# Performance work log

Measured on AMD Instinct MI355X. Metric: run time of the kernel, lower is better.

The kernel has to match this reference:

```python
import jax, jax.numpy as jnp
import numpy as np

DIM = 1024
NUM_HEADS = 16
HEAD_DIM = DIM // NUM_HEADS
EPS = 1e-6


def _xavier(key, shape, gain=0.1):
    fan_in, fan_out = shape[1], shape[0]
    limit = gain * np.sqrt(6.0 / (fan_in + fan_out))
    return jax.random.uniform(key, shape, jnp.float32, -limit, limit)


def setup_inputs() -> dict:
    key = jax.random.key(0)
    kx, kq, kk, kv, ko = jax.random.split(key, 5)
    B, N = 4, 4096
    return {
        "x": jax.random.normal(kx, (B, N, DIM), jnp.float32),
        "Wq": _xavier(kq, (DIM, DIM)), "bq": jnp.zeros((DIM,), jnp.float32),
        "Wk": _xavier(kk, (DIM, DIM)), "bk": jnp.zeros((DIM,), jnp.float32),
        "Wv": _xavier(kv, (DIM, DIM)), "bv": jnp.zeros((DIM,), jnp.float32),
        "Wo": _xavier(ko, (DIM, DIM)), "bo": jnp.zeros((DIM,), jnp.float32),
    }


def _phi(x):
    # ELU feature map: elu(x) + 1 ensures non-negativity
    return jax.nn.elu(x) + 1.0


def reference(x, Wq, bq, Wk, bk, Wv, bv, Wo, bo):
    B, N, D = x.shape
    H, Hd = NUM_HEADS, HEAD_DIM
    # torch Linear: y = x @ W.T + b
    Q = (x @ Wq.T + bq).reshape(B, N, H, Hd).transpose(0, 2, 1, 3)
    K = (x @ Wk.T + bk).reshape(B, N, H, Hd).transpose(0, 2, 1, 3)
    V = (x @ Wv.T + bv).reshape(B, N, H, Hd).transpose(0, 2, 1, 3)
    Q = _phi(Q)
    K = _phi(K)
    KV = jnp.einsum('bhnd,bhne->bhde', K, V)          # [B,H,Hd,Hd] state
    out = jnp.einsum('bhnd,bhde->bhne', Q, KV)        # [B,H,N,Hd]
    Z = K.sum(axis=2)                                  # [B,H,Hd]
    norm = jnp.einsum('bhnd,bhd->bhn', Q, Z)[..., None] + EPS
    out = out / norm
    out = out.transpose(0, 2, 1, 3).reshape(B, N, D)
    return out @ Wo.T + bo
```

## Files before the change

### kernel.cpp

```cpp
#include <hip/hip_runtime.h>
#include <math.h>

#define DIMC 1024
#define SEQ 4096
#define BATCH 4
#define NH 16
#define HD 64
#define MTOT (BATCH * SEQ)
#define NSPLIT 8
#define PELEMS (64 * 64 * 64 + 64 * 64)
#define EPS 1e-6f
#define NKT (DIMC / 64)

typedef __bf16 bf16x8 __attribute__((ext_vector_type(8)));
typedef __bf16 bf16x4 __attribute__((ext_vector_type(4)));
typedef __bf16 bf16x2 __attribute__((ext_vector_type(2)));
typedef float  f32x4  __attribute__((ext_vector_type(4)));

#define MFMA16 __builtin_amdgcn_mfma_f32_16x16x32_bf16

__device__ __forceinline__ float phi_f(float x) {
    return x > 0.0f ? x + 1.0f : __expf(x);
}

__global__ __launch_bounds__(256) void cvt_all(
    const float* __restrict__ x,
    const float* __restrict__ Wq, const float* __restrict__ Wk,
    const float* __restrict__ Wv, const float* __restrict__ Wo,
    __bf16* __restrict__ xb,
    __bf16* __restrict__ Wqb, __bf16* __restrict__ Wkb,
    __bf16* __restrict__ Wvb, __bf16* __restrict__ Wob)
{
    const size_t big = (size_t)MTOT * DIMC;
    const size_t wsz = (size_t)DIMC * DIMC;
    size_t i = ((size_t)blockIdx.x * 256 + threadIdx.x) * 4;
    const float* src; __bf16* dst; size_t off;
    if (i < big) { src = x; dst = xb; off = i; }
    else {
        size_t j = i - big;
        int w = (int)(j >> 20);
        off = j & (wsz - 1);
        switch (w) {
            case 0: src = Wq; dst = Wqb; break;
            case 1: src = Wk; dst = Wkb; break;
            case 2: src = Wv; dst = Wvb; break;
            default: src = Wo; dst = Wob; break;
        }
    }
    float4 v = *(const float4*)(src + off);
    bf16x4 o = { (__bf16)v.x, (__bf16)v.y, (__bf16)v.z, (__bf16)v.w };
    *(bf16x4*)(dst + off) = o;
}

template<int OUT_BF16>
__device__ __forceinline__ void gemm_tile256(
    const __bf16* __restrict__ X, const __bf16* __restrict__ W,
    const float* __restrict__ bias, void* __restrict__ Yv,
    int m0, int n0, int do_phi)
{
    __shared__ __attribute__((aligned(16))) __bf16 lds[65536];
    const int tid  = threadIdx.x;
    const int wave = tid >> 6, lane = tid & 63;
    const int wm = wave >> 2, wn = wave & 3;
    const int fr = lane & 15, fkb = lane >> 4;
    const int fsw = fr & 7;
    const int srow = lane >> 3;
    const int sblk = (lane & 7) ^ srow;

    const __bf16* Asrc = X + (size_t)(m0 + wave * 8 + srow) * DIMC + sblk * 8;
    const __bf16* Bsrc = W + (size_t)(n0 + wave * 8 + srow) * DIMC + sblk * 8;
    __bf16* lw = lds + wave * 512;

    auto stage = [&](int isB, int h, int kblk, int bb) {
        const __bf16* s = (isB ? Bsrc : Asrc)
                          + (size_t)(h * 128) * DIMC + (size_t)kblk * 64;
        __bf16* d = lw + bb * 32768 + isB * 16384 + h * 8192;
        #pragma unroll
        for (int g = 0; g < 2; ++g)
            __builtin_amdgcn_global_load_lds(
                (const __attribute__((address_space(1))) void*)(s + (size_t)g * 64 * DIMC),
                (__attribute__((address_space(3))) void*)(d + g * 4096),
                16, 0, 0);
    };
    auto lda = [&](int bb, int i, int ks) -> bf16x8 {
        return *(const bf16x8*)(lds + bb * 32768 + wm * 8192
                 + (i * 16 + fr) * 64 + (((ks * 4 + fkb) ^ fsw) * 8));
    };
    auto ldb = [&](int bb, int j, int ks) -> bf16x8 {
        return *(const bf16x8*)(lds + bb * 32768 + 16384 + (wn >> 1) * 8192
                 + ((wn & 1) * 64 + j * 16 + fr) * 64 + (((ks * 4 + fkb) ^ fsw) * 8));
    };

    f32x4 acc[8][4] = {};
    bf16x8 a[4][2], b[4][2];

    stage(1, 0, 0, 0); stage(1, 1, 0, 0);
    stage(0, 0, 0, 0); stage(0, 1, 0, 0);
    stage(1, 0, 1, 1); stage(1, 1, 1, 1);
    stage(0, 0, 1, 1);
    asm volatile("s_waitcnt vmcnt(6)" ::: "memory");
    __builtin_amdgcn_s_barrier();

    #pragma unroll 2
    for (int t = 0; t < NKT; ++t) {
        const int buf = t & 1;
        #pragma unroll
        for (int i = 0; i < 4; ++i)
            #pragma unroll
            for (int ks = 0; ks < 2; ++ks) a[i][ks] = lda(buf, i, ks);
        #pragma unroll
        for (int j = 0; j < 2; ++j)
            #pragma unroll
            for (int ks = 0; ks < 2; ++ks) b[j][ks] = ldb(buf, j, ks);
        if (t + 1 < NKT) stage(0, 1, t + 1, buf ^ 1);
        __builtin_amdgcn_s_barrier();
        asm volatile("s_waitcnt lgkmcnt(0)" ::: "memory");
        __builtin_amdgcn_s_setprio(1);
        #pragma unroll
        for (int i = 0; i < 4; ++i)
            #pragma unroll
            for (int j = 0; j < 2; ++j)
                #pragma unroll
                for (int ks = 0; ks < 2; ++ks)
                    acc[i][j] = MFMA16(a[i][ks], b[j][ks], acc[i][j], 0, 0, 0);
        __builtin_amdgcn_s_setprio(0);
        __builtin_amdgcn_s_barrier();
        #pragma unroll
        for (int j = 2; j < 4; ++j)
            #pragma unroll
            for (int ks = 0; ks < 2; ++ks) b[j][ks] = ldb(buf, j, ks);
        __builtin_amdgcn_s_barrier();
        asm volatile("s_waitcnt lgkmcnt(0)" ::: "memory");
        __builtin_amdgcn_s_setprio(1);
        #pragma unroll
        for (int i = 0; i < 4; ++i)
            #pragma unroll
            for (int j = 2; j < 4; ++j)
                #pragma unroll
                for (int ks = 0; ks < 2; ++ks)
                    acc[i][j] = MFMA16(a[i][ks], b[j][ks], acc[i][j], 0, 0, 0);
        __builtin_amdgcn_s_setprio(0);
        __builtin_amdgcn_s_barrier();
        #pragma unroll
        for (int i = 0; i < 4; ++i)
            #pragma unroll
            for (int ks = 0; ks < 2; ++ks) a[i][ks] = lda(buf, i + 4, ks);
        if (t + 2 < NKT) stage(1, 0, t + 2, buf);
        __builtin_amdgcn_s_barrier();
        asm volatile("s_waitcnt lgkmcnt(0)" ::: "memory");
        __builtin_amdgcn_s_setprio(1);
        #pragma unroll
        for (int i = 0; i < 4; ++i)
            #pragma unroll
            for (int j = 2; j < 4; ++j)
                #pragma unroll
                for (int ks = 0; ks < 2; ++ks)
                    acc[i + 4][j] = MFMA16(a[i][ks], b[j][ks], acc[i + 4][j], 0, 0, 0);
        __builtin_amdgcn_s_setprio(0);
        __builtin_amdgcn_s_barrier();
        if (t + 2 < NKT) {
            stage(1, 1, t + 2, buf);
            stage(0, 0, t + 2, buf);
        }
        __builtin_amdgcn_s_setprio(1);
        #pragma unroll
        for (int i = 0; i < 4; ++i)
            #pragma unroll
            for (int j = 0; j < 2; ++j)
                #pragma unroll
                for (int ks = 0; ks < 2; ++ks)
                    acc[i + 4][j] = MFMA16(a[i][ks], b[j][ks], acc[i + 4][j], 0, 0, 0);
        __builtin_amdgcn_s_setprio(0);
        if (t < NKT - 2)       asm volatile("s_waitcnt vmcnt(6)" ::: "memory");
        else if (t == NKT - 2) asm volatile("s_waitcnt vmcnt(0)" ::: "memory");
        __builtin_amdgcn_s_barrier();
    }

    const int col_l = lane & 15, quad = lane >> 4;
    const int cbase = n0 + wn * 64 + col_l;
    float bb4[4];
    #pragma unroll
    for (int j = 0; j < 4; ++j) bb4[j] = bias[cbase + j * 16];
    #pragma unroll
    for (int i = 0; i < 8; ++i) {
        #pragma unroll
        for (int r = 0; r < 4; ++r) {
            const size_t grow = (size_t)(m0 + wm * 128 + i * 16 + quad * 4 + r) * DIMC;
            #pragma unroll
            for (int j = 0; j < 4; ++j) {
                float v = acc[i][j][r] + bb4[j];
                if (do_phi) v = phi_f(v);
                if (OUT_BF16)
                    ((__bf16*)Yv)[grow + cbase + j * 16] = (__bf16)v;
                else
                    ((float*)Yv)[grow + cbase + j * 16] = v;
            }
        }
    }
}

__global__ __launch_bounds__(512, 2) void gemm_qkv(
    const __bf16* __restrict__ X,
    const __bf16* __restrict__ Wq, const __bf16* __restrict__ Wk,
    const __bf16* __restrict__ Wv,
    const float* __restrict__ bq, const float* __restrict__ bk,
    const float* __restrict__ bv,
    __bf16* __restrict__ Q, __bf16* __restrict__ K, __bf16* __restrict__ V)
{
    const int l = blockIdx.x;
    const int xcd = l & 7, s = l >> 3;
    const int mat = s >> 5;
    const int t = s & 31;
    const int nb = t & 3;
    const int m_idx = xcd * 8 + (t >> 2);
    const __bf16* W = (mat == 0) ? Wq : (mat == 1) ? Wk : Wv;
    const float* bias = (mat == 0) ? bq : (mat == 1) ? bk : bv;
    __bf16* Y = (mat == 0) ? Q : (mat == 1) ? K : V;
    gemm_tile256<1>(X, W, bias, (void*)Y, m_idx * 256, nb * 256, mat != 2);
}

__global__ __launch_bounds__(512, 2) void gemm_out(
    const __bf16* __restrict__ A, const __bf16* __restrict__ Wo,
    const float* __restrict__ bo, float* __restrict__ out)
{
    const int l = blockIdx.x;
    const int xcd = l & 7, s = l >> 3;
    const int m_idx = xcd * 8 + (s >> 2);
    const int nb = s & 3;
    gemm_tile256<0>(A, Wo, bo, (void*)out, m_idx * 256, nb * 256, 0);
}

__global__ __launch_bounds__(256) void kv_z_kernel(
    const __bf16* __restrict__ Kb, const __bf16* __restrict__ Vb,
    float* __restrict__ P)
{
    __shared__ __attribute__((aligned(16))) __bf16 Kt[2][64 * 36];
    __shared__ __attribute__((aligned(16))) __bf16 Vt[2][64 * 36];
    __shared__ float zs[64];
    const int tid = threadIdx.x, wave = tid >> 6, lane = tid & 63;
    const int bh = blockIdx.x, b = bh >> 4, h = bh & 15;
    const int split = blockIdx.y;
    const int n0 = split * (SEQ / NSPLIT);
    const int dg = (tid & 15) * 4;
    const int u2 = (tid >> 4) * 2;
    const int fr = lane & 15, fk = (lane >> 4) * 8;
    const __bf16* Kp = Kb + ((size_t)b * SEQ + n0) * DIMC + h * HD;
    const __bf16* Vp = Vb + ((size_t)b * SEQ + n0) * DIMC + h * HD;
    constexpr int CH = (SEQ / NSPLIT) / 32;

    if (tid < 64) zs[tid] = 0.0f;
    f32x4 acc[4] = {};
    float zp[4] = {};

    auto ldc = [&](int c, bf16x4& ka, bf16x4& kb, bf16x4& va, bf16x4& vb) {
        ka = *(const bf16x4*)(Kp + (size_t)(c * 32 + u2) * DIMC + dg);
        kb = *(const bf16x4*)(Kp + (size_t)(c * 32 + u2 + 1) * DIMC + dg);
        va = *(const bf16x4*)(Vp + (size_t)(c * 32 + u2) * DIMC + dg);
        vb = *(const bf16x4*)(Vp + (size_t)(c * 32 + u2 + 1) * DIMC + dg);
    };

    bf16x4 ka, kb, va, vb;
    ldc(0, ka, kb, va, vb);

    for (int c = 0; c < CH; ++c) {
        const int p = c & 1;
        #pragma unroll
        for (int q = 0; q < 4; ++q) {
            zp[q] += (float)ka[q] + (float)kb[q];
            *(bf16x2*)(Kt[p] + (dg + q) * 36 + u2) = bf16x2{ka[q], kb[q]};
            *(bf16x2*)(Vt[p] + (dg + q) * 36 + u2) = bf16x2{va[q], vb[q]};
        }
        bf16x4 nka, nkb, nva, nvb;
        if (c + 1 < CH) ldc(c + 1, nka, nkb, nva, nvb);
        __syncthreads();

        const __bf16* ar = Kt[p] + (wave * 16 + fr) * 36 + fk;
        bf16x4 alo = *(const bf16x4*)ar, ahi = *(const bf16x4*)(ar + 4);
        bf16x8 af = {alo[0],alo[1],alo[2],alo[3],ahi[0],ahi[1],ahi[2],ahi[3]};
        #pragma unroll
        for (int j = 0; j < 4; ++j) {
            const __bf16* br = Vt[p] + (j * 16 + fr) * 36 + fk;
            bf16x4 blo = *(const bf16x4*)br, bhi = *(const bf16x4*)(br + 4);
            bf16x8 bf = {blo[0],blo[1],blo[2],blo[3],bhi[0],bhi[1],bhi[2],bhi[3]};
            acc[j] = __builtin_amdgcn_mfma_f32_16x16x32_bf16(af, bf, acc[j], 0, 0, 0);
        }
        ka = nka; kb = nkb; va = nva; vb = nvb;
    }

    #pragma unroll
    for (int q = 0; q < 4; ++q) atomicAdd(&zs[dg + q], zp[q]);
    __syncthreads();

    float* KVp = P + (size_t)split * PELEMS + bh * 4096;
    const int col_l = lane & 15, quad = lane >> 4;
    #pragma unroll
    for (int j = 0; j < 4; ++j)
        #pragma unroll
        for (int r = 0; r < 4; ++r)
            KVp[(wave * 16 + quad * 4 + r) * 64 + j * 16 + col_l] = acc[j][r];
    if (tid < 64)
        P[(size_t)split * PELEMS + 64 * 64 * 64 + bh * 64 + tid] = zs[tid];
}

__global__ __launch_bounds__(256) void reduce_partials(
    const float* __restrict__ P, float* __restrict__ F)
{
    const int i = blockIdx.x * 256 + threadIdx.x;
    if (i < PELEMS) {
        float s = 0.0f;
        #pragma unroll
        for (int sp = 0; sp < NSPLIT; ++sp) s += P[(size_t)sp * PELEMS + i];
        F[i] = s;
    }
}

__global__ __launch_bounds__(256) void attn_apply(
    const __bf16* __restrict__ Qb, const float* __restrict__ KV,
    const float* __restrict__ Z, __bf16* __restrict__ Ab)
{
    __shared__ __align__(16) float KVs[64][64];
    __shared__ __align__(16) float Qs[32][64];
    __shared__ float Zs[64];
    __shared__ float rnorm[32];
    const int tid = threadIdx.x;
    const int bh = blockIdx.y;
    const int b = bh >> 4, h = bh & 15;
    const int n0 = blockIdx.x * 32;

    const float* KVp = KV + (size_t)bh * HD * HD;
    #pragma unroll
    for (int r = 0; r < 4; ++r) {
        const int idx = (r * 256 + tid) * 4;
        *(float4*)&((float*)KVs)[idx] = *(const float4*)(KVp + idx);
    }
    const __bf16* Qp = Qb + ((size_t)(b * SEQ + n0)) * DIMC + h * HD;
    {
        const int tok = tid >> 3, col = (tid & 7) * 8;
        bf16x8 q8 = *(const bf16x8*)(Qp + (size_t)tok * DIMC + col);
        #pragma unroll
        for (int q = 0; q < 8; ++q) Qs[tok][col + q] = (float)q8[q];
    }
    if (tid < 64) Zs[tid] = Z[bh * HD + tid];
    __syncthreads();

    if (tid < 32) {
        float s = 0.0f;
        #pragma unroll
        for (int d = 0; d < 64; ++d) s += Qs[tid][d] * Zs[d];
        rnorm[tid] = 1.0f / (s + EPS);
    }
    __syncthreads();

    const int trow = tid >> 3;
    const int e0 = (tid & 7) * 8;
    float out[8] = {};
    #pragma unroll
    for (int d = 0; d < 64; ++d) {
        const float q = Qs[trow][d];
        #pragma unroll
        for (int j = 0; j < 8; ++j) out[j] = fmaf(q, KVs[d][e0 + j], out[j]);
    }
    const float rn = rnorm[trow];
    __bf16* Op = Ab + ((size_t)(b * SEQ + n0 + trow)) * DIMC + h * HD + e0;
    bf16x8 o;
    #pragma unroll
    for (int j = 0; j < 8; ++j) o[j] = (__bf16)(out[j] * rn);
    *(bf16x8*)Op = o;
}

extern "C" void kernel_launch(void* const* d_in, const int* in_sizes, int n_in,
                              void* d_out, int out_size, void* d_ws, size_t ws_size,
                              hipStream_t stream) {
    const float* x  = (const float*)d_in[0];
    const float* Wq = (const float*)d_in[1];
    const float* bq = (const float*)d_in[2];
    const float* Wk = (const float*)d_in[3];
    const float* bk = (const float*)d_in[4];
    const float* Wv = (const float*)d_in[5];
    const float* bv = (const float*)d_in[6];
    const float* Wo = (const float*)d_in[7];
    const float* bo = (const float*)d_in[8];
    float* out = (float*)d_out;

    const size_t big = (size_t)MTOT * DIMC;
    const size_t wsz = (size_t)DIMC * DIMC;
    __bf16* wsp = (__bf16*)d_ws;
    __bf16* xb  = wsp;
    __bf16* Wqb = xb + big;
    __bf16* Wkb = Wqb + wsz;
    __bf16* Wvb = Wkb + wsz;
    __bf16* Wob = Wvb + wsz;
    __bf16* Qb  = Wob + wsz;
    __bf16* Kb  = Qb + big;
    __bf16* Vb  = Kb + big;
    __bf16* Ab  = xb;
    float*  P   = (float*)(Vb + big);
    float*  F   = P + (size_t)NSPLIT * PELEMS;
    float*  KV  = F;
    float*  Z   = F + 64 * 64 * 64;

    const size_t ntot = big + 4 * wsz;
    cvt_all<<<dim3((int)(ntot / 1024)), 256, 0, stream>>>(
        x, Wq, Wk, Wv, Wo, xb, Wqb, Wkb, Wvb, Wob);

    gemm_qkv<<<dim3(768), 512, 0, stream>>>(
        xb, Wqb, Wkb, Wvb, bq, bk, bv, Qb, Kb, Vb);

    kv_z_kernel<<<dim3(BATCH * NH, NSPLIT), 256, 0, stream>>>(Kb, Vb, P);
    reduce_partials<<<dim3((PELEMS + 255) / 256), 256, 0, stream>>>(P, F);
    attn_apply<<<dim3(SEQ / 32, BATCH * NH), 256, 0, stream>>>(Qb, KV, Z, Ab);

    gemm_out<<<dim3(256), 512, 0, stream>>>(Ab, Wob, bo, out);
}
```

Measured before the change: 342.4 us.

## Shrink GEMM tiles to 128x128 with 4 waves and fuse attn norm via shuffles

```diff
diff --git a/kernel.cpp b/kernel.cpp
--- a/kernel.cpp
+++ b/kernel.cpp
@@ -53,51 +53,47 @@
 }
 
 template<int OUT_BF16>
-__device__ __forceinline__ void gemm_tile256(
+__device__ __forceinline__ void gemm_tile128(
     const __bf16* __restrict__ X, const __bf16* __restrict__ W,
     const float* __restrict__ bias, void* __restrict__ Yv,
     int m0, int n0, int do_phi)
 {
-    __shared__ __attribute__((aligned(16))) __bf16 lds[65536];
+    __shared__ __attribute__((aligned(16))) __bf16 lds[32768];
     const int tid  = threadIdx.x;
     const int wave = tid >> 6, lane = tid & 63;
-    const int wm = wave >> 2, wn = wave & 3;
+    const int wm = wave >> 1, wn = wave & 1;
     const int fr = lane & 15, fkb = lane >> 4;
     const int fsw = fr & 7;
     const int srow = lane >> 3;
-    const int sblk = (lane & 7) ^ srow;
+    const int sblk = (lane & 7) ^ (srow & 7);
 
     const __bf16* Asrc = X + (size_t)(m0 + wave * 8 + srow) * DIMC + sblk * 8;
     const __bf16* Bsrc = W + (size_t)(n0 + wave * 8 + srow) * DIMC + sblk * 8;
-    __bf16* lw = lds + wave * 512;
-
-    auto stage = [&](int isB, int h, int kblk, int bb) {
+
+    auto stage = [&](int isB, int q, int kblk, int bb) {
         const __bf16* s = (isB ? Bsrc : Asrc)
-                          + (size_t)(h * 128) * DIMC + (size_t)kblk * 64;
-        __bf16* d = lw + bb * 32768 + isB * 16384 + h * 8192;
-        #pragma unroll
-        for (int g = 0; g < 2; ++g)
-            __builtin_amdgcn_global_load_lds(
-                (const __attribute__((address_space(1))) void*)(s + (size_t)g * 64 * DIMC),
-                (__attribute__((address_space(3))) void*)(d + g * 4096),
-                16, 0, 0);
+                          + (size_t)(q * 32) * DIMC + (size_t)kblk * 64;
+        __bf16* d = lds + bb * 16384 + isB * 8192 + q * 2048 + wave * 512;
+        __builtin_amdgcn_global_load_lds(
+            (const __attribute__((address_space(1))) void*)s,
+            (__attribute__((address_space(3))) void*)d, 16, 0, 0);
     };
     auto lda = [&](int bb, int i, int ks) -> bf16x8 {
-        return *(const bf16x8*)(lds + bb * 32768 + wm * 8192
-                 + (i * 16 + fr) * 64 + (((ks * 4 + fkb) ^ fsw) * 8));
+        return *(const bf16x8*)(lds + bb * 16384
+                 + (wm * 64 + i * 16 + fr) * 64 + (((ks * 4 + fkb) ^ fsw) * 8));
     };
     auto ldb = [&](int bb, int j, int ks) -> bf16x8 {
-        return *(const bf16x8*)(lds + bb * 32768 + 16384 + (wn >> 1) * 8192
-                 + ((wn & 1) * 64 + j * 16 + fr) * 64 + (((ks * 4 + fkb) ^ fsw) * 8));
+        return *(const bf16x8*)(lds + bb * 16384 + 8192
+                 + (wn * 64 + j * 16 + fr) * 64 + (((ks * 4 + fkb) ^ fsw) * 8));
     };
 
-    f32x4 acc[8][4] = {};
-    bf16x8 a[4][2], b[4][2];
-
-    stage(1, 0, 0, 0); stage(1, 1, 0, 0);
-    stage(0, 0, 0, 0); stage(0, 1, 0, 0);
-    stage(1, 0, 1, 1); stage(1, 1, 1, 1);
-    stage(0, 0, 1, 1);
+    f32x4 acc[4][4] = {};
+    bf16x8 a[2][2], b[4][2];
+
+    stage(1, 0, 0, 0); stage(1, 1, 0, 0); stage(1, 2, 0, 0); stage(1, 3, 0, 0);
+    stage(0, 0, 0, 0); stage(0, 1, 0, 0); stage(0, 2, 0, 0); stage(0, 3, 0, 0);
+    stage(1, 0, 1, 1); stage(1, 1, 1, 1); stage(1, 2, 1, 1); stage(1, 3, 1, 1);
+    stage(0, 0, 1, 1); stage(0, 1, 1, 1);
     asm volatile("s_waitcnt vmcnt(6)" ::: "memory");
     __builtin_amdgcn_s_barrier();
 
@@ -105,19 +101,19 @@
     for (int t = 0; t < NKT; ++t) {
         const int buf = t & 1;
         #pragma unroll
-        for (int i = 0; i < 4; ++i)
+        for (int i = 0; i < 2; ++i)
             #pragma unroll
             for (int ks = 0; ks < 2; ++ks) a[i][ks] = lda(buf, i, ks);
         #pragma unroll
         for (int j = 0; j < 2; ++j)
             #pragma unroll
             for (int ks = 0; ks < 2; ++ks) b[j][ks] = ldb(buf, j, ks);
-        if (t + 1 < NKT) stage(0, 1, t + 1, buf ^ 1);
+        if (t + 1 < NKT) { stage(0, 2, t + 1, buf ^ 1); stage(0, 3, t + 1, buf ^ 1); }
         __builtin_amdgcn_s_barrier();
         asm volatile("s_waitcnt lgkmcnt(0)" ::: "memory");
         __builtin_amdgcn_s_setprio(1);
         #pragma unroll
-        for (int i = 0; i < 4; ++i)
+        for (int i = 0; i < 2; ++i)
             #pragma unroll
             for (int j = 0; j < 2; ++j)
                 #pragma unroll
@@ -133,7 +129,7 @@
         asm volatile("s_waitcnt lgkmcnt(0)" ::: "memory");
         __builtin_amdgcn_s_setprio(1);
         #pragma unroll
-        for (int i = 0; i < 4; ++i)
+        for (int i = 0; i < 2; ++i)
             #pragma unroll
             for (int j = 2; j < 4; ++j)
                 #pragma unroll
@@ -142,34 +138,34 @@
         __builtin_amdgcn_s_setprio(0);
         __builtin_amdgcn_s_barrier();
         #pragma unroll
-        for (int i = 0; i < 4; ++i)
-            #pragma unroll
-            for (int ks = 0; ks < 2; ++ks) a[i][ks] = lda(buf, i + 4, ks);
-        if (t + 2 < NKT) stage(1, 0, t + 2, buf);
+        for (int i = 0; i < 2; ++i)
+            #pragma unroll
+            for (int ks = 0; ks < 2; ++ks) a[i][ks] = lda(buf, i + 2, ks);
+        if (t + 2 < NKT) { stage(1, 0, t + 2, buf); stage(1, 1, t + 2, buf); }
         __builtin_amdgcn_s_barrier();
         asm volatile("s_waitcnt lgkmcnt(0)" ::: "memory");
         __builtin_amdgcn_s_setprio(1);
         #pragma unroll
-        for (int i = 0; i < 4; ++i)
+        for (int i = 0; i < 2; ++i)
             #pragma unroll
             for (int j = 2; j < 4; ++j)
                 #pragma unroll
                 for (int ks = 0; ks < 2; ++ks)
-                    acc[i + 4][j] = MFMA16(a[i][ks], b[j][ks], acc[i + 4][j], 0, 0, 0);
+                    acc[i + 2][j] = MFMA16(a[i][ks], b[j][ks], acc[i + 2][j], 0, 0, 0);
         __builtin_amdgcn_s_setprio(0);
         __builtin_amdgcn_s_barrier();
         if (t + 2 < NKT) {
-            stage(1, 1, t + 2, buf);
-            stage(0, 0, t + 2, buf);
+            stage(1, 2, t + 2, buf); stage(1, 3, t + 2, buf);
+            stage(0, 0, t + 2, buf); stage(0, 1, t + 2, buf);
         }
         __builtin_amdgcn_s_setprio(1);
         #pragma unroll
-        for (int i = 0; i < 4; ++i)
+        for (int i = 0; i < 2; ++i)
             #pragma unroll
             for (int j = 0; j < 2; ++j)
                 #pragma unroll
                 for (int ks = 0; ks < 2; ++ks)
-                    acc[i + 4][j] = MFMA16(a[i][ks], b[j][ks], acc[i + 4][j], 0, 0, 0);
+                    acc[i + 2][j] = MFMA16(a[i][ks], b[j][ks], acc[i + 2][j], 0, 0, 0);
         __builtin_amdgcn_s_setprio(0);
         if (t < NKT - 2)       asm volatile("s_waitcnt vmcnt(6)" ::: "memory");
         else if (t == NKT - 2) asm volatile("s_waitcnt vmcnt(0)" ::: "memory");
@@ -182,10 +178,10 @@
     #pragma unroll
     for (int j = 0; j < 4; ++j) bb4[j] = bias[cbase + j * 16];
     #pragma unroll
-    for (int i = 0; i < 8; ++i) {
+    for (int i = 0; i < 4; ++i) {
         #pragma unroll
         for (int r = 0; r < 4; ++r) {
-            const size_t grow = (size_t)(m0 + wm * 128 + i * 16 + quad * 4 + r) * DIMC;
+            const size_t grow = (size_t)(m0 + wm * 64 + i * 16 + quad * 4 + r) * DIMC;
             #pragma unroll
             for (int j = 0; j < 4; ++j) {
                 float v = acc[i][j][r] + bb4[j];
@@ -199,7 +195,7 @@
     }
 }
 
-__global__ __launch_bounds__(512, 2) void gemm_qkv(
+__global__ __launch_bounds__(256, 2) void gemm_qkv(
     const __bf16* __restrict__ X,
     const __bf16* __restrict__ Wq, const __bf16* __restrict__ Wk,
     const __bf16* __restrict__ Wv,
@@ -209,25 +205,25 @@
 {
     const int l = blockIdx.x;
     const int xcd = l & 7, s = l >> 3;
-    const int mat = s >> 5;
-    const int t = s & 31;
-    const int nb = t & 3;
-    const int m_idx = xcd * 8 + (t >> 2);
+    const int mat = s >> 7;
+    const int t = s & 127;
+    const int nb = t & 7;
+    const int m_idx = xcd * 16 + (t >> 3);
     const __bf16* W = (mat == 0) ? Wq : (mat == 1) ? Wk : Wv;
     const float* bias = (mat == 0) ? bq : (mat == 1) ? bk : bv;
     __bf16* Y = (mat == 0) ? Q : (mat == 1) ? K : V;
-    gemm_tile256<1>(X, W, bias, (void*)Y, m_idx * 256, nb * 256, mat != 2);
-}
-
-__global__ __launch_bounds__(512, 2) void gemm_out(
+    gemm_tile128<1>(X, W, bias, (void*)Y, m_idx * 128, nb * 128, mat != 2);
+}
+
+__global__ __launch_bounds__(256, 2) void gemm_out(
     const __bf16* __restrict__ A, const __bf16* __restrict__ Wo,
     const float* __restrict__ bo, float* __restrict__ out)
 {
     const int l = blockIdx.x;
     const int xcd = l & 7, s = l >> 3;
-    const int m_idx = xcd * 8 + (s >> 2);
-    const int nb = s & 3;
-    gemm_tile256<0>(A, Wo, bo, (void*)out, m_idx * 256, nb * 256, 0);
+    const int nb = s & 7;
+    const int m_idx = xcd * 16 + (s >> 3);
+    gemm_tile128<0>(A, Wo, bo, (void*)out, m_idx * 128, nb * 128, 0);
 }
 
 __global__ __launch_bounds__(256) void kv_z_kernel(
@@ -320,8 +316,6 @@
 {
     __shared__ __align__(16) float KVs[64][64];
     __shared__ __align__(16) float Qs[32][64];
-    __shared__ float Zs[64];
-    __shared__ float rnorm[32];
     const int tid = threadIdx.x;
     const int bh = blockIdx.y;
     const int b = bh >> 4, h = bh & 15;
@@ -333,26 +327,27 @@
         const int idx = (r * 256 + tid) * 4;
         *(float4*)&((float*)KVs)[idx] = *(const float4*)(KVp + idx);
     }
-    const __bf16* Qp = Qb + ((size_t)(b * SEQ + n0)) * DIMC + h * HD;
-    {
-        const int tok = tid >> 3, col = (tid & 7) * 8;
-        bf16x8 q8 = *(const bf16x8*)(Qp + (size_t)tok * DIMC + col);
-        #pragma unroll
-        for (int q = 0; q < 8; ++q) Qs[tok][col + q] = (float)q8[q];
-    }
-    if (tid < 64) Zs[tid] = Z[bh * HD + tid];
-    __syncthreads();
-
-    if (tid < 32) {
-        float s = 0.0f;
-        #pragma unroll
-        for (int d = 0; d < 64; ++d) s += Qs[tid][d] * Zs[d];
-        rnorm[tid] = 1.0f / (s + EPS);
-    }
-    __syncthreads();
-
     const int trow = tid >> 3;
     const int e0 = (tid & 7) * 8;
+    const __bf16* Qp = Qb + ((size_t)(b * SEQ + n0)) * DIMC + h * HD;
+    float part = 0.0f;
+    {
+        bf16x8 q8 = *(const bf16x8*)(Qp + (size_t)trow * DIMC + e0);
+        const float* Zp = Z + bh * HD + e0;
+        float4 z0 = *(const float4*)Zp, z1 = *(const float4*)(Zp + 4);
+        float zf[8] = {z0.x, z0.y, z0.z, z0.w, z1.x, z1.y, z1.z, z1.w};
+        #pragma unroll
+        for (int q = 0; q < 8; ++q) {
+            const float qv = (float)q8[q];
+            Qs[trow][e0 + q] = qv;
+            part = fmaf(qv, zf[q], part);
+        }
+    }
+    #pragma unroll
+    for (int m = 1; m < 8; m <<= 1) part += __shfl_xor(part, m);
+    const float rn = 1.0f / (part + EPS);
+    __syncthreads();
+
     float out[8] = {};
     #pragma unroll
     for (int d = 0; d < 64; ++d) {
@@ -360,7 +355,6 @@
         #pragma unroll
         for (int j = 0; j < 8; ++j) out[j] = fmaf(q, KVs[d][e0 + j], out[j]);
     }
-    const float rn = rnorm[trow];
     __bf16* Op = Ab + ((size_t)(b * SEQ + n0 + trow)) * DIMC + h * HD + e0;
     bf16x8 o;
     #pragma unroll
@@ -403,12 +397,12 @@
     cvt_all<<<dim3((int)(ntot / 1024)), 256, 0, stream>>>(
         x, Wq, Wk, Wv, Wo, xb, Wqb, Wkb, Wvb, Wob);
 
-    gemm_qkv<<<dim3(768), 512, 0, stream>>>(
+    gemm_qkv<<<dim3(3072), 256, 0, stream>>>(
         xb, Wqb, Wkb, Wvb, bq, bk, bv, Qb, Kb, Vb);
 
     kv_z_kernel<<<dim3(BATCH * NH, NSPLIT), 256, 0, stream>>>(Kb, Vb, P);
     reduce_partials<<<dim3((PELEMS + 255) / 256), 256, 0, stream>>>(P, F);
     attn_apply<<<dim3(SEQ / 32, BATCH * NH), 256, 0, stream>>>(Qb, KV, Z, Ab);
 
-    gemm_out<<<dim3(256), 512, 0, stream>>>(Ab, Wob, bo, out);
-}
+    gemm_out<<<dim3(1024), 256, 0, stream>>>(Ab, Wob, bo, out);
+}
```

Result: slower. 349.8 us (+2.2%).

## Use MFMA with split-bf16 KV in attn_apply and process 128 tokens per block

Applied to the files above, without the earlier changes.

```diff
diff --git a/kernel.cpp b/kernel.cpp
--- a/kernel.cpp
+++ b/kernel.cpp
@@ -315,57 +315,98 @@
 }
 
 __global__ __launch_bounds__(256) void attn_apply(
-    const __bf16* __restrict__ Qb, const float* __restrict__ KV,
-    const float* __restrict__ Z, __bf16* __restrict__ Ab)
-{
-    __shared__ __align__(16) float KVs[64][64];
-    __shared__ __align__(16) float Qs[32][64];
-    __shared__ float Zs[64];
-    __shared__ float rnorm[32];
-    const int tid = threadIdx.x;
-    const int bh = blockIdx.y;
-    const int b = bh >> 4, h = bh & 15;
-    const int n0 = blockIdx.x * 32;
-
-    const float* KVp = KV + (size_t)bh * HD * HD;
+    const __bf16* __restrict__ Qb, const float* __restrict__ F,
+    __bf16* __restrict__ Ab)
+{
+    __shared__ __align__(16) float  Ftmp[4096];
+    __shared__ __align__(16) __bf16 KVhi[64 * 80];
+    __shared__ __align__(16) __bf16 KVlo[64 * 80];
+    __shared__ __align__(16) __bf16 Qs[128 * 80];
+    const int tid = threadIdx.x, wave = tid >> 6, lane = tid & 63;
+    const int bhh = blockIdx.y, b = bhh >> 4, h = bhh & 15;
+    const int n0 = blockIdx.x * 128;
+
+    const float* KVp = F + (size_t)bhh * 4096;
     #pragma unroll
     for (int r = 0; r < 4; ++r) {
         const int idx = (r * 256 + tid) * 4;
-        *(float4*)&((float*)KVs)[idx] = *(const float4*)(KVp + idx);
+        *(float4*)&Ftmp[idx] = *(const float4*)(KVp + idx);
     }
     const __bf16* Qp = Qb + ((size_t)(b * SEQ + n0)) * DIMC + h * HD;
+    const int qrow = tid >> 3, qcol = (tid & 7) * 8;
+    bf16x8 qv[4];
+    #pragma unroll
+    for (int rr = 0; rr < 4; ++rr)
+        qv[rr] = *(const bf16x8*)(Qp + (size_t)(rr * 32 + qrow) * DIMC + qcol);
+    __syncthreads();
+
     {
-        const int tok = tid >> 3, col = (tid & 7) * 8;
-        bf16x8 q8 = *(const bf16x8*)(Qp + (size_t)tok * DIMC + col);
-        #pragma unroll
-        for (int q = 0; q < 8; ++q) Qs[tok][col + q] = (float)q8[q];
-    }
-    if (tid < 64) Zs[tid] = Z[bh * HD + tid];
+        const int e = tid >> 2, d0 = (tid & 3) * 16;
+        #pragma unroll
+        for (int k = 0; k < 16; k += 2) {
+            float v0 = Ftmp[(d0 + k) * 64 + e];
+            float v1 = Ftmp[(d0 + k + 1) * 64 + e];
+            __bf16 h0 = (__bf16)v0, h1 = (__bf16)v1;
+            *(bf16x2*)(KVhi + e * 80 + d0 + k) = bf16x2{h0, h1};
+            *(bf16x2*)(KVlo + e * 80 + d0 + k) =
+                bf16x2{(__bf16)(v0 - (float)h0), (__bf16)(v1 - (float)h1)};
+        }
+        #pragma unroll
+        for (int rr = 0; rr < 4; ++rr)
+            *(bf16x8*)(Qs + (rr * 32 + qrow) * 80 + qcol) = qv[rr];
+    }
     __syncthreads();
 
-    if (tid < 32) {
-        float s = 0.0f;
-        #pragma unroll
-        for (int d = 0; d < 64; ++d) s += Qs[tid][d] * Zs[d];
-        rnorm[tid] = 1.0f / (s + EPS);
-    }
-    __syncthreads();
-
-    const int trow = tid >> 3;
-    const int e0 = (tid & 7) * 8;
-    float out[8] = {};
-    #pragma unroll
-    for (int d = 0; d < 64; ++d) {
-        const float q = Qs[trow][d];
-        #pragma unroll
-        for (int j = 0; j < 8; ++j) out[j] = fmaf(q, KVs[d][e0 + j], out[j]);
-    }
-    const float rn = rnorm[trow];
-    __bf16* Op = Ab + ((size_t)(b * SEQ + n0 + trow)) * DIMC + h * HD + e0;
-    bf16x8 o;
-    #pragma unroll
-    for (int j = 0; j < 8; ++j) o[j] = (__bf16)(out[j] * rn);
-    *(bf16x8*)Op = o;
+    const int tt = lane & 31, half = lane >> 5;
+    float part = 0.0f;
+    const float* Zp = F + 64 * 64 * 64 + bhh * HD + half * 32;
+    #pragma unroll
+    for (int g = 0; g < 4; ++g) {
+        bf16x8 q8 = *(const bf16x8*)(Qs + (wave * 32 + tt) * 80 + half * 32 + g * 8);
+        float4 z0 = *(const float4*)(Zp + g * 8);
+        float4 z1 = *(const float4*)(Zp + g * 8 + 4);
+        part = fmaf((float)q8[0], z0.x, part);
+        part = fmaf((float)q8[1], z0.y, part);
+        part = fmaf((float)q8[2], z0.z, part);
+        part = fmaf((float)q8[3], z0.w, part);
+        part = fmaf((float)q8[4], z1.x, part);
+        part = fmaf((float)q8[5], z1.y, part);
+        part = fmaf((float)q8[6], z1.z, part);
+        part = fmaf((float)q8[7], z1.w, part);
+    }
+    part += __shfl_xor(part, 32);
+    const float rn = 1.0f / (part + EPS);
+
+    const int fr = lane & 15, fkb = lane >> 4;
+    f32x4 acc[2][4] = {};
+    #pragma unroll
+    for (int ks = 0; ks < 2; ++ks) {
+        bf16x8 a0 = *(const bf16x8*)(Qs + (wave * 32 + fr) * 80 + ks * 32 + fkb * 8);
+        bf16x8 a1 = *(const bf16x8*)(Qs + (wave * 32 + 16 + fr) * 80 + ks * 32 + fkb * 8);
+        #pragma unroll
+        for (int j = 0; j < 4; ++j) {
+            bf16x8 bh8 = *(const bf16x8*)(KVhi + (j * 16 + fr) * 80 + ks * 32 + fkb * 8);
+            bf16x8 bl8 = *(const bf16x8*)(KVlo + (j * 16 + fr) * 80 + ks * 32 + fkb * 8);
+            acc[0][j] = MFMA16(a0, bh8, acc[0][j], 0, 0, 0);
+            acc[0][j] = MFMA16(a0, bl8, acc[0][j], 0, 0, 0);
+            acc[1][j] = MFMA16(a1, bh8, acc[1][j], 0, 0, 0);
+            acc[1][j] = MFMA16(a1, bl8, acc[1][j], 0, 0, 0);
+        }
+    }
+
+    const int col_l = lane & 15, quad = lane >> 4;
+    #pragma unroll
+    for (int i = 0; i < 2; ++i) {
+        #pragma unroll
+        for (int r = 0; r < 4; ++r) {
+            const float rni = __shfl(rn, i * 16 + quad * 4 + r);
+            const int tok = n0 + wave * 32 + i * 16 + quad * 4 + r;
+            __bf16* Op = Ab + ((size_t)(b * SEQ + tok)) * DIMC + h * HD + col_l;
+            #pragma unroll
+            for (int j = 0; j < 4; ++j)
+                Op[j * 16] = (__bf16)(acc[i][j][r] * rni);
+        }
+    }
 }
 
 extern "C" void kernel_launch(void* const* d_in, const int* in_sizes, int n_in,
@@ -396,8 +437,6 @@
     __bf16* Ab  = xb;
     float*  P   = (float*)(Vb + big);
     float*  F   = P + (size_t)NSPLIT * PELEMS;
-    float*  KV  = F;
-    float*  Z   = F + 64 * 64 * 64;
 
     const size_t ntot = big + 4 * wsz;
     cvt_all<<<dim3((int)(ntot / 1024)), 256, 0, stream>>>(
@@ -408,7 +447,7 @@
 
     kv_z_kernel<<<dim3(BATCH * NH, NSPLIT), 256, 0, stream>>>(Kb, Vb, P);
     reduce_partials<<<dim3((PELEMS + 255) / 256), 256, 0, stream>>>(P, F);
-    attn_apply<<<dim3(SEQ / 32, BATCH * NH), 256, 0, stream>>>(Qb, KV, Z, Ab);
+    attn_apply<<<dim3(SEQ / 128, BATCH * NH), 256, 0, stream>>>(Qb, F, Ab);
 
     gemm_out<<<dim3(256), 512, 0, stream>>>(Ab, Wob, bo, out);
 }
```

After: 302.2 us. 11.7% less time.
